# Kernel optimization log

Measured on AMD Instinct MI355X. Metric: run time of the kernel, lower is better.

The kernel has to match this reference:

```python
import jax, jax.numpy as jnp
import numpy as np

EPS = 1e-5
KS = 3
PAD = 1


def _bn(x, g, b, m, v):
    inv = g / jnp.sqrt(v + EPS)
    return x * inv[None, :, None, None] + (b - m * inv)[None, :, None, None]


def _deform_conv2d(x, off_w, off_b, w):
    # x: (B,C,H,W); off_w: (2*9,C,3,3); w: (Cout,C,3,3)
    B, C, H, W = x.shape
    N = KS * KS
    off = jax.lax.conv_general_dilated(x, off_w, (1, 1), ((PAD, PAD), (PAD, PAD)))
    off = off + off_b[None, :, None, None]                      # (B,2N,H,W)
    xp = jnp.pad(x, ((0, 0), (0, 0), (PAD, PAD), (PAD, PAD)))
    Hp, Wp = H + 2 * PAD, W + 2 * PAD
    r = jnp.arange(KS, dtype=x.dtype) - (KS - 1) // 2           # kernel offsets
    pny = jnp.repeat(r, KS)                                     # row-major (dy)
    pnx = jnp.tile(r, KS)                                       # row-major (dx)
    p0y = jnp.arange(1, H + 1, dtype=x.dtype)[None, None, :, None]
    p0x = jnp.arange(1, W + 1, dtype=x.dtype)[None, None, None, :]
    py = off[:, :N] + pny[None, :, None, None] + p0y            # (B,N,H,W)
    px = off[:, N:] + pnx[None, :, None, None] + p0x
    py = jnp.clip(py, 0.0, Hp - 1.0)
    px = jnp.clip(px, 0.0, Wp - 1.0)
    fy = jax.lax.stop_gradient(jnp.floor(py))                   # indices detached (as in torch impl)
    fx = jax.lax.stop_gradient(jnp.floor(px))
    qy0 = jnp.clip(fy, 0.0, Hp - 1.0)
    qx0 = jnp.clip(fx, 0.0, Wp - 1.0)
    qy1 = jnp.clip(fy + 1.0, 0.0, Hp - 1.0)
    qx1 = jnp.clip(fx + 1.0, 0.0, Wp - 1.0)
    xf = xp.reshape(B, C, Hp * Wp)

    def gather(qy, qx):
        idx = (qy * Wp + qx).astype(jnp.int32)                  # (B,N,H,W)
        return jax.vmap(lambda m_, i_: m_[:, i_])(xf, idx)       # (B,C,N,H,W)

    g_lt = (1.0 + (qy0 - py)) * (1.0 + (qx0 - px))
    g_rb = (1.0 - (qy1 - py)) * (1.0 - (qx1 - px))
    g_lb = (1.0 + (qy0 - py)) * (1.0 - (qx1 - px))
    g_rt = (1.0 - (qy1 - py)) * (1.0 + (qx0 - px))
    xo = (g_lt[:, None] * gather(qy0, qx0) + g_rb[:, None] * gather(qy1, qx1)
          + g_lb[:, None] * gather(qy0, qx1) + g_rt[:, None] * gather(qy1, qx0))
    # (B,C,N,H,W) -> (B,C,H*KS,W*KS): N = (row, col) row-major
    xo = xo.reshape(B, C, KS, KS, H, W).transpose(0, 1, 4, 2, 5, 3).reshape(B, C, H * KS, W * KS)
    return jax.lax.conv_general_dilated(xo, w, (KS, KS), 'VALID')


def _forward(x, dc1_offw, dc1_offb, dc1_w, bn1_g, bn1_b, bn1_m, bn1_v,
             dc2_offw, dc2_offb, dc2_w, bn2_g, bn2_b, bn2_m, bn2_v,
             id_w, id_b, bn3_g, bn3_b, bn3_m, bn3_v):
    h = jax.nn.relu(_bn(_deform_conv2d(x, dc1_offw, dc1_offb, dc1_w), bn1_g, bn1_b, bn1_m, bn1_v))
    h = _bn(_deform_conv2d(h, dc2_offw, dc2_offb, dc2_w), bn2_g, bn2_b, bn2_m, bn2_v)
    idt = jnp.einsum('bchw,oc->bohw', x, id_w[:, :, 0, 0]) + id_b[None, :, None, None]
    idt = _bn(idt, bn3_g, bn3_b, bn3_m, bn3_v)
    return jax.nn.relu(h + idt)


def setup_inputs() -> dict:
    key = jax.random.key(0)
    ks = jax.random.split(key, 16)
    B, Cin, Cout, H, W = 2, 64, 128, 128, 128
    N2 = 2 * KS * KS
    d = {}
    d['x'] = jax.random.normal(ks[0], (B, Cin, H, W), jnp.float32)
    d['dc1_offw'] = jax.random.normal(ks[1], (N2, Cin, KS, KS), jnp.float32) * 0.01
    d['dc1_offb'] = jnp.zeros((N2,), jnp.float32)
    d['dc1_w'] = jax.random.normal(ks[2], (Cout, Cin, KS, KS), jnp.float32) * 0.05
    d['bn1_g'] = 1.0 + 0.1 * jax.random.normal(ks[3], (Cout,), jnp.float32)
    d['bn1_b'] = 0.1 * jax.random.normal(ks[4], (Cout,), jnp.float32)
    d['bn1_m'] = 0.1 * jax.random.normal(ks[5], (Cout,), jnp.float32)
    d['bn1_v'] = jnp.ones((Cout,), jnp.float32)
    d['dc2_offw'] = jax.random.normal(ks[6], (N2, Cout, KS, KS), jnp.float32) * 0.01
    d['dc2_offb'] = jnp.zeros((N2,), jnp.float32)
    d['dc2_w'] = jax.random.normal(ks[7], (Cout, Cout, KS, KS), jnp.float32) * 0.03
    d['bn2_g'] = 1.0 + 0.1 * jax.random.normal(ks[8], (Cout,), jnp.float32)
    d['bn2_b'] = 0.1 * jax.random.normal(ks[9], (Cout,), jnp.float32)
    d['bn2_m'] = 0.1 * jax.random.normal(ks[10], (Cout,), jnp.float32)
    d['bn2_v'] = jnp.ones((Cout,), jnp.float32)
    d['id_w'] = jax.random.normal(ks[11], (Cout, Cin, 1, 1), jnp.float32) * 0.1
    d['id_b'] = jnp.zeros((Cout,), jnp.float32)
    d['bn3_g'] = 1.0 + 0.1 * jax.random.normal(ks[12], (Cout,), jnp.float32)
    d['bn3_b'] = 0.1 * jax.random.normal(ks[13], (Cout,), jnp.float32)
    d['bn3_m'] = 0.1 * jax.random.normal(ks[14], (Cout,), jnp.float32)
    d['bn3_v'] = jnp.ones((Cout,), jnp.float32)
    return d


def reference(x, dc1_offw, dc1_offb, dc1_w, bn1_g, bn1_b, bn1_m, bn1_v,
              dc2_offw, dc2_offb, dc2_w, bn2_g, bn2_b, bn2_m, bn2_v,
              id_w, id_b, bn3_g, bn3_b, bn3_m, bn3_v):
    return _forward(x, dc1_offw, dc1_offb, dc1_w, bn1_g, bn1_b, bn1_m, bn1_v,
                    dc2_offw, dc2_offb, dc2_w, bn2_g, bn2_b, bn2_m, bn2_v,
                    id_w, id_b, bn3_g, bn3_b, bn3_m, bn3_v)
```

## Files before the change

kernel.cpp:

```cpp
#include <hip/hip_runtime.h>
#include <math.h>

#define HH 128
#define WW 128
#define HWSZ (HH * WW)
#define BB 2
#define COUT 128

typedef __bf16 bf16x8 __attribute__((ext_vector_type(8)));
typedef float f32x4 __attribute__((ext_vector_type(4)));
typedef float f32x2 __attribute__((ext_vector_type(2)));
typedef short s16x8 __attribute__((ext_vector_type(8)));
typedef short s16x4 __attribute__((ext_vector_type(4)));
typedef unsigned short u16x4 __attribute__((ext_vector_type(4)));
typedef unsigned short u16x8 __attribute__((ext_vector_type(8)));

__device__ __forceinline__ short tobf(float f) {
  union { float f; unsigned u; } v; v.f = f;
  unsigned r = v.u + 0x7fffu + ((v.u >> 16) & 1u);
  return (short)(r >> 16);
}
__device__ __forceinline__ float asf(unsigned u) {
  union { unsigned u; float f; } v; v.u = u;
  return v.f;
}
__device__ __forceinline__ f32x2 up2(unsigned u) {
  f32x2 r; r[0] = asf(u << 16); r[1] = asf(u & 0xffff0000u); return r;
}
__device__ __forceinline__ unsigned trunc2bf(f32x2 v) {
  union { float f; unsigned u; } a, b;
  a.f = v[0]; b.f = v[1];
  return __builtin_amdgcn_perm(b.u, a.u, 0x07060302u);
}

#define PA0 73728
#define PA1 221184
#define PA2 229376
#define PA3 247808
#define PA4 284672
#define PA5 284928
__global__ __launch_bounds__(256) void prep_all_kernel(
    const float* __restrict__ dc1_w, const float* __restrict__ dc2_w,
    const float* __restrict__ id_w, const float* __restrict__ dc1_offw,
    const float* __restrict__ dc2_offw,
    const float* g1, const float* b1, const float* m1, const float* v1,
    const float* g2, const float* b2, const float* m2, const float* v2,
    const float* g3, const float* b3, const float* m3, const float* v3,
    const float* idb,
    short* __restrict__ wbf1, short* __restrict__ wbf2,
    short* __restrict__ woff1, short* __restrict__ woff2,
    float* __restrict__ cb1, float* __restrict__ cb2) {
  int idx = blockIdx.x * 256 + threadIdx.x;
  if (idx < PA0) {
    int o = idx / 576, k = idx - o * 576;
    float inv = g1[o] / sqrtf(v1[o] + 1e-5f);
    int col = (k % 9) * 64 + k / 9;
    int di = (((col >> 5) * 2 + (o >> 6)) * 4 + ((o >> 4) & 3)) * 512
           + (((o & 15) | (((col >> 3) & 3) << 4)) * 8) + (col & 7);
    wbf1[di] = tobf(dc1_w[(size_t)o * 576 + k] * inv);
  } else if (idx < PA1) {
    int j = idx - PA0;
    int o = j / 1152, k = j - o * 1152;
    float inv = g2[o] / sqrtf(v2[o] + 1e-5f);
    int col = (k % 9) * 128 + k / 9;
    int di = (((col >> 5) * 2 + (o >> 6)) * 4 + ((o >> 4) & 3)) * 512
           + (((o & 15) | (((col >> 3) & 3) << 4)) * 8) + (col & 7);
    wbf2[di] = tobf(dc2_w[(size_t)o * 1152 + k] * inv);
  } else if (idx < PA2) {
    int j = idx - PA1;
    int o = j >> 6, k = j & 63;
    float inv = g3[o] / sqrtf(v3[o] + 1e-5f);
    int col = 1152 + k;
    int di = (((col >> 5) * 2 + (o >> 6)) * 4 + ((o >> 4) & 3)) * 512
           + (((o & 15) | (((col >> 3) & 3) << 4)) * 8) + (col & 7);
    wbf2[di] = tobf(id_w[(size_t)o * 64 + k] * inv);
  } else if (idx < PA3) {
    int j = idx - PA2;
    int o = j / 576, k = j - o * 576;
    int col = (k % 9) * 64 + k / 9;
    int di = ((col >> 5) * 2 + (o >> 4)) * 512 + ((col >> 3) & 3) * 128
           + (o & 15) * 8 + (col & 7);
    woff1[di] = (o < 18) ? tobf(dc1_offw[(size_t)o * 576 + k]) : (short)0;
  } else if (idx < PA4) {
    int j = idx - PA3;
    int o = j / 1152, k = j - o * 1152;
    int col = (k % 9) * 128 + k / 9;
    int di = ((col >> 5) * 2 + (o >> 4)) * 512 + ((col >> 3) & 3) * 128
           + (o & 15) * 8 + (col & 7);
    woff2[di] = (o < 18) ? tobf(dc2_offw[(size_t)o * 1152 + k]) : (short)0;
  } else if (idx < PA5) {
    int j = idx - PA4;
    if (j < 128) {
      float inv = g1[j] / sqrtf(v1[j] + 1e-5f);
      cb1[j] = b1[j] - m1[j] * inv;
    } else {
      int o = j - 128;
      float inv2_ = g2[o] / sqrtf(v2[o] + 1e-5f);
      float inv3_ = g3[o] / sqrtf(v3[o] + 1e-5f);
      cb2[o] = (b2[o] - m2[o] * inv2_) + idb[o] * inv3_ + (b3[o] - m3[o] * inv3_);
    }
  }
}

__global__ __launch_bounds__(256) void xcast_kernel(const float* __restrict__ x,
                                                    unsigned short* __restrict__ xn) {
  __shared__ short lds[64 * 72];
  int tid = threadIdx.x;
  int gp0 = blockIdx.x * 64;
  int b = gp0 >> 14;
  int pl0 = gp0 & 16383;
  int p = tid & 63;
  int cb = (tid >> 6) * 16;
#pragma unroll
  for (int i = 0; i < 16; i++) {
    int c = cb + i;
    lds[p * 72 + c] = tobf(x[((size_t)(b * 64 + c)) * HWSZ + pl0 + p]);
  }
  __syncthreads();
  int pw = tid >> 2, cseg = (tid & 3) * 16;
  u16x8 a = *(const u16x8*)&lds[pw * 72 + cseg];
  u16x8 b8 = *(const u16x8*)&lds[pw * 72 + cseg + 8];
  *(u16x8*)&xn[(size_t)(gp0 + pw) * 64 + cseg] = a;
  *(u16x8*)&xn[(size_t)(gp0 + pw) * 64 + cseg + 8] = b8;
}

#define LOADW(kc_)                                              \
  {                                                             \
    const short* wf_ = wfb + (size_t)(kc_) * 4096;              \
    w0 = *(const bf16x8*)(wf_);                                 \
    w1 = *(const bf16x8*)(wf_ + 512);                           \
    w2 = *(const bf16x8*)(wf_ + 1024);                          \
    w3 = *(const bf16x8*)(wf_ + 1536);                          \
    w4 = *(const bf16x8*)(wf_ + 2048);                          \
    w5 = *(const bf16x8*)(wf_ + 2560);                          \
    w6 = *(const bf16x8*)(wf_ + 3072);                          \
    w7 = *(const bf16x8*)(wf_ + 3584);                          \
  }

#define LOADD(kc_)                                              \
  {                                                             \
    int n_ = ((kc_) << 5) >> CSH;                               \
    Dd0 = dsu[(n_ << 5) + dp];                                  \
  }

#define LOADG(P, kc_)                                           \
  {                                                             \
    int k0_ = (kc_) << 5;                                       \
    int c0_ = (k0_ & (Cin - 1)) + cq * 8;                       \
    int dx_ = (int)(Dd0.w & 0xffffu);                           \
    int dy_ = (int)Dd0.w >> 16;                                 \
    const unsigned short* p_ = inb + (int)Dd0.z + c0_;          \
    P##q00 = *(const uint4*)(p_);                               \
    P##q01 = *(const uint4*)(p_ + dx_);                         \
    P##q02 = *(const uint4*)(p_ + dy_);                         \
    P##q03 = *(const uint4*)(p_ + dx_ + dy_);                   \
    P##wa0 = Dd0.x; P##wb0 = Dd0.y;                             \
  }

#define BLEND1(r0, r1, r2, r3, wav, wbv, pkv)                                 \
  {                                                                           \
    float w0_ = asf((wav) << 16), w1_ = asf((wav) & 0xffff0000u);             \
    float w2_ = asf((wbv) << 16), w3_ = asf((wbv) & 0xffff0000u);             \
    f32x2 v0_ = up2(r0.x) * w0_ + up2(r1.x) * w1_                             \
              + up2(r2.x) * w2_ + up2(r3.x) * w3_;                            \
    f32x2 v1_ = up2(r0.y) * w0_ + up2(r1.y) * w1_                             \
              + up2(r2.y) * w2_ + up2(r3.y) * w3_;                            \
    f32x2 v2_ = up2(r0.z) * w0_ + up2(r1.z) * w1_                             \
              + up2(r2.z) * w2_ + up2(r3.z) * w3_;                            \
    f32x2 v3_ = up2(r0.w) * w0_ + up2(r1.w) * w1_                             \
              + up2(r2.w) * w2_ + up2(r3.w) * w3_;                            \
    pkv.x = trunc2bf(v0_); pkv.y = trunc2bf(v1_);                             \
    pkv.z = trunc2bf(v2_); pkv.w = trunc2bf(v3_);                             \
  }

#define XPOSE(pkv, bfrv)                                                      \
  {                                                                           \
    union { int i[4]; bf16x8 v; } bu_;                                        \
    bu_.i[0] = __builtin_amdgcn_ds_bpermute(baddr, (int)pkv.x);               \
    bu_.i[1] = __builtin_amdgcn_ds_bpermute(baddr, (int)pkv.y);               \
    bu_.i[2] = __builtin_amdgcn_ds_bpermute(baddr, (int)pkv.z);               \
    bu_.i[3] = __builtin_amdgcn_ds_bpermute(baddr, (int)pkv.w);               \
    bfrv = bu_.v;                                                             \
  }

#define MFMA8(bfr0v)                                                                \
  {                                                                                 \
    acc[0] = __builtin_amdgcn_mfma_f32_16x16x32_bf16(w0, bfr0v, acc[0], 0, 0, 0);   \
    acc[1] = __builtin_amdgcn_mfma_f32_16x16x32_bf16(w1, bfr0v, acc[1], 0, 0, 0);   \
    acc[2] = __builtin_amdgcn_mfma_f32_16x16x32_bf16(w2, bfr0v, acc[2], 0, 0, 0);   \
    acc[3] = __builtin_amdgcn_mfma_f32_16x16x32_bf16(w3, bfr0v, acc[3], 0, 0, 0);   \
    acc[4] = __builtin_amdgcn_mfma_f32_16x16x32_bf16(w4, bfr0v, acc[4], 0, 0, 0);   \
    acc[5] = __builtin_amdgcn_mfma_f32_16x16x32_bf16(w5, bfr0v, acc[5], 0, 0, 0);   \
    acc[6] = __builtin_amdgcn_mfma_f32_16x16x32_bf16(w6, bfr0v, acc[6], 0, 0, 0);   \
    acc[7] = __builtin_amdgcn_mfma_f32_16x16x32_bf16(w7, bfr0v, acc[7], 0, 0, 0);   \
  }

#define COMPUTE(P)                                                            \
  {                                                                           \
    uint4 pk0_;                                                               \
    BLEND1(P##q00, P##q01, P##q02, P##q03, P##wa0, P##wb0, pk0_);             \
    bf16x8 bf0_;                                                              \
    XPOSE(pk0_, bf0_);                                                        \
    __builtin_amdgcn_s_setprio(1);                                            \
    MFMA8(bf0_);                                                              \
    __builtin_amdgcn_s_setprio(0);                                            \
  }

template <int CSH, int KCONV, int KTOT, int MODE>
__global__ __launch_bounds__(256, 3) void fused_layer_kernel(
    const unsigned short* __restrict__ in, const short* __restrict__ woff,
    const float* __restrict__ offb,
    const short* __restrict__ wbf, const float* __restrict__ cbv,
    const unsigned short* __restrict__ xid, float* __restrict__ outf,
    unsigned short* __restrict__ outb) {
  __shared__ __align__(16) char smem[25088];
  uint4* dsu = (uint4*)smem;
  f32x4* redf = (f32x4*)smem;
  float* offlds = (float*)(smem + 16384);
  short* trans = (short*)(smem + 16384);

  const int tid = threadIdx.x;
  const int lane = tid & 63, wv = tid >> 6;
  const int pb = ((blockIdx.x & 7) << 7) | (blockIdx.x >> 3);
  const int pix0 = pb << 5;
  const int pl = pix0 & 16383;
  const int x0 = pl & 127, y = pl >> 7, b = pix0 >> 14;
  constexpr int Cin = 1 << CSH;
  const unsigned short* inb = in + (size_t)b * HWSZ * Cin;
  const int l15 = lane & 15, quad = lane >> 4;
  const int pxa = wv & 1, kh = wv >> 1;
  const int dp = pxa * 16 + (lane >> 2);
  const int cq = lane & 3;
  const int baddr = (((lane & 15) << 2) | (lane >> 4)) << 2;

  if (wv < 2) {
    constexpr int NCh = (9 << CSH) >> 5;
    const int pxga = wv;
    const int px = x0 + pxga * 16 + l15;
    f32x4 aco0 = {0.f, 0.f, 0.f, 0.f};
    f32x4 aco1 = {0.f, 0.f, 0.f, 0.f};
#pragma unroll
    for (int i = 0; i < NCh; i++) {
      int k0 = i * 32;
      int n = k0 >> CSH;
      int c0 = (k0 & (Cin - 1)) + quad * 8;
      int yy = y + n / 3 - 1;
      int xx = px + n % 3 - 1;
      bf16x8 bv = {};
      if (((unsigned)yy < (unsigned)HH) && ((unsigned)xx < (unsigned)WW))
        bv = *(const bf16x8*)&inb[((size_t)yy * WW + xx) * Cin + c0];
      int fbase = i * 1024 + lane * 8;
      bf16x8 a0 = *(const bf16x8*)&woff[fbase];
      bf16x8 a1 = *(const bf16x8*)&woff[fbase + 512];
      aco0 = __builtin_amdgcn_mfma_f32_16x16x32_bf16(a0, bv, aco0, 0, 0, 0);
      aco1 = __builtin_amdgcn_mfma_f32_16x16x32_bf16(a1, bv, aco1, 0, 0, 0);
    }
#pragma unroll
    for (int r = 0; r < 4; r++) {
      int o0 = quad * 4 + r;
      offlds[o0 * 32 + pxga * 16 + l15] = aco0[r] + offb[o0];
      int o1 = 16 + quad * 4 + r;
      if (o1 < 18)
        offlds[o1 * 32 + pxga * 16 + l15] = aco1[r] + offb[o1];
    }
  }

  bf16x8 w0, w1, w2, w3, w4, w5, w6, w7;
  uint4 Aq00, Aq01, Aq02, Aq03;
  uint4 Bq00, Bq01, Bq02, Bq03;
  unsigned Awa0, Awb0, Bwa0, Bwb0;
  uint4 Dd0;

  constexpr int NC = KTOT >> 5;
  constexpr int NCONV = KCONV >> 5;
  const int kcBeg = (NC * kh) >> 1;
  const int kcEnd = (NC * (kh + 1)) >> 1;
  const int kcEndConv = (kcEnd < NCONV) ? kcEnd : NCONV;
  const short* wfb = wbf + lane * 8;

  __syncthreads();

  for (int t = tid; t < 288; t += 256) {
    int n = t >> 5, pp = t & 31;
    float offy = offlds[n * 32 + pp];
    float offx = offlds[(9 + n) * 32 + pp];
    float py = offy + (float)(n / 3 - 1) + (float)(y + 1);
    float px = offx + (float)(n % 3 - 1) + (float)(x0 + pp + 1);
    py = fminf(fmaxf(py, 0.f), 129.f);
    px = fminf(fmaxf(px, 0.f), 129.f);
    float fy = floorf(py), fx = floorf(px);
    float qy1 = fminf(fy + 1.f, 129.f), qx1 = fminf(fx + 1.f, 129.f);
    float ty0 = 1.f + fy - py, ty1 = 1.f - (qy1 - py);
    float tx0 = 1.f + fx - px, tx1 = 1.f - (qx1 - px);
    int iy0 = (int)fy - 1, ix0 = (int)fx - 1;
    int iy1 = (int)qy1 - 1, ix1 = (int)qx1 - 1;
    if ((unsigned)iy0 >= (unsigned)HH) ty0 = 0.f;
    if ((unsigned)iy1 >= (unsigned)HH) ty1 = 0.f;
    if ((unsigned)ix0 >= (unsigned)WW) tx0 = 0.f;
    if ((unsigned)ix1 >= (unsigned)WW) tx1 = 0.f;
    int by0 = min(max(iy0, 0), HH - 1), by1 = min(max(iy1, 0), HH - 1);
    int bx0 = min(max(ix0, 0), WW - 1), bx1 = min(max(ix1, 0), WW - 1);
    uint4 d4;
    d4.x = (unsigned)(unsigned short)tobf(ty0 * tx0)
         | ((unsigned)(unsigned short)tobf(ty0 * tx1) << 16);
    d4.y = (unsigned)(unsigned short)tobf(ty1 * tx0)
         | ((unsigned)(unsigned short)tobf(ty1 * tx1) << 16);
    d4.z = (unsigned)((by0 * WW + bx0) * Cin);
    d4.w = (unsigned)((((by1 - by0) * WW * Cin) << 16) | ((bx1 - bx0) * Cin));
    dsu[t] = d4;
  }

  f32x4 acc[8];
#pragma unroll
  for (int j = 0; j < 8; j++) acc[j] = (f32x4){0.f, 0.f, 0.f, 0.f};

  __syncthreads();

  int i = kcBeg;
  if (i < kcEndConv) {
    const int kcLast = kcEndConv - 1;
    LOADD(i);
    LOADG(A, i);
    LOADD(min(i + 1, kcLast));
    for (; i + 2 <= kcEndConv; i += 2) {
      LOADW(i);
      LOADG(B, i + 1);
      LOADD(min(i + 2, kcLast));
      COMPUTE(A);
      LOADW(i + 1);
      if (i + 2 < kcEndConv) {
        LOADG(A, i + 2);
        LOADD(min(i + 3, kcLast));
      }
      COMPUTE(B);
    }
    if (i < kcEndConv) {
      LOADW(i);
      COMPUTE(A);
      i++;
    }
  }

  if (KCONV < KTOT) {
    for (; i < kcEnd; i++) {
      LOADW(i);
      int c = ((i << 5) - KCONV) + cq * 8;
      uint4 pk0 = *(const uint4*)&xid[((size_t)(b * HWSZ) + y * WW + x0 + dp) * 64 + c];
      bf16x8 bf0;
      XPOSE(pk0, bf0);
      __builtin_amdgcn_s_setprio(1);
      MFMA8(bf0);
      __builtin_amdgcn_s_setprio(0);
    }
  }

  __syncthreads();
  if (kh == 1) {
#pragma unroll
    for (int f = 0; f < 8; f++) redf[(f * 2 + pxa) * 64 + lane] = acc[f];
  }
  __syncthreads();
  if (kh == 0) {
#pragma unroll
    for (int f = 0; f < 8; f++) acc[f] += redf[(f * 2 + pxa) * 64 + lane];
    if (MODE == 1) {
#pragma unroll
      for (int f = 0; f < 8; f++) {
        int px_ = x0 + pxa * 16 + l15;
#pragma unroll
        for (int r = 0; r < 4; r++) {
          int o = (f >> 2) * 64 + (f & 3) * 16 + quad * 4 + r;
          outf[(size_t)(b * COUT + o) * HWSZ + y * WW + px_] =
              fmaxf(acc[f][r] + cbv[o], 0.f);
        }
      }
    } else {
#pragma unroll
      for (int f = 0; f < 8; f++) {
        int pl_ = pxa * 16 + l15;
        s16x4 t4;
#pragma unroll
        for (int r = 0; r < 4; r++) {
          int o = (f >> 2) * 64 + (f & 3) * 16 + quad * 4 + r;
          t4[r] = tobf(fmaxf(acc[f][r] + cbv[o], 0.f));
        }
        *(s16x4*)&trans[pl_ * 136 + (f >> 2) * 64 + (f & 3) * 16 + quad * 4] = t4;
      }
    }
  }
  if (MODE == 0) {
    __syncthreads();
    int pw = tid >> 3, cs = (tid & 7) * 16;
    size_t gb = ((size_t)(b * HWSZ) + y * WW + x0 + pw) * 128 + cs;
#pragma unroll
    for (int s = 0; s < 2; s++) {
      u16x8 v8 = *(const u16x8*)&trans[pw * 136 + cs + s * 8];
      *(u16x8*)&outb[gb + s * 8] = v8;
    }
  }
}

extern "C" void kernel_launch(void* const* d_in, const int* in_sizes, int n_in,
                              void* d_out, int out_size, void* d_ws, size_t ws_size,
                              hipStream_t stream) {
  const float* x        = (const float*)d_in[0];
  const float* dc1_offw = (const float*)d_in[1];
  const float* dc1_offb = (const float*)d_in[2];
  const float* dc1_w    = (const float*)d_in[3];
  const float* bn1_g    = (const float*)d_in[4];
  const float* bn1_b    = (const float*)d_in[5];
  const float* bn1_m    = (const float*)d_in[6];
  const float* bn1_v    = (const float*)d_in[7];
  const float* dc2_offw = (const float*)d_in[8];
  const float* dc2_offb = (const float*)d_in[9];
  const float* dc2_w    = (const float*)d_in[10];
  const float* bn2_g    = (const float*)d_in[11];
  const float* bn2_b    = (const float*)d_in[12];
  const float* bn2_m    = (const float*)d_in[13];
  const float* bn2_v    = (const float*)d_in[14];
  const float* id_w     = (const float*)d_in[15];
  const float* id_b     = (const float*)d_in[16];
  const float* bn3_g    = (const float*)d_in[17];
  const float* bn3_b    = (const float*)d_in[18];
  const float* bn3_m    = (const float*)d_in[19];
  const float* bn3_v    = (const float*)d_in[20];

  float* wsf = (float*)d_ws;
  float* cb1  = wsf;
  float* cb2  = cb1 + 128;
  unsigned short* xbf = (unsigned short*)(cb2 + 128);
  unsigned short* h1  = xbf + (size_t)BB * HWSZ * 64;
  short* wbf1  = (short*)(h1 + (size_t)BB * HWSZ * COUT);
  short* wbf2  = wbf1 + (size_t)128 * 576;
  short* woff1 = wbf2 + (size_t)128 * 1216;
  short* woff2 = woff1 + (size_t)18 * 1024;

  hipLaunchKernelGGL(prep_all_kernel, dim3((PA5 + 255) / 256), dim3(256), 0, stream,
                     dc1_w, dc2_w, id_w, dc1_offw, dc2_offw,
                     bn1_g, bn1_b, bn1_m, bn1_v, bn2_g, bn2_b, bn2_m, bn2_v,
                     bn3_g, bn3_b, bn3_m, bn3_v, id_b,
                     wbf1, wbf2, woff1, woff2, cb1, cb2);
  hipLaunchKernelGGL(xcast_kernel, dim3(BB * HWSZ / 64), dim3(256), 0, stream, x, xbf);

  hipLaunchKernelGGL((fused_layer_kernel<6, 576, 576, 0>), dim3(1024), dim3(256), 0, stream,
                     xbf, woff1, dc1_offb, wbf1, cb1,
                     (const unsigned short*)nullptr, (float*)nullptr, h1);
  hipLaunchKernelGGL((fused_layer_kernel<7, 1152, 1216, 1>), dim3(1024), dim3(256), 0, stream,
                     h1, woff2, dc2_offb, wbf2, cb2,
                     xbf, (float*)d_out, (unsigned short*)nullptr);
}
```

Measured before the change: 188.8 us.

## Triple-buffer deformable gather loads in conv main loop

Replaces the two-stage A/B register double buffering of gathered input samples with a three-stage A/B/C rotation, so gathers run two chunks ahead of the MFMA compute. The K-split between the two halves changes so each half gets exactly half of the conv chunks, with the identity tail going to the second half. The intent is to hide gather latency better. The cost is higher register pressure, and the loop requires the chunk count per half to be a multiple of three or the remainder is silently dropped.

Measured after the change: 186.9 us. About the same (-1.0%).

```diff
diff --git a/kernel.cpp b/kernel.cpp
--- a/kernel.cpp
+++ b/kernel.cpp
@@ -268,14 +268,16 @@
   bf16x8 w0, w1, w2, w3, w4, w5, w6, w7;
   uint4 Aq00, Aq01, Aq02, Aq03;
   uint4 Bq00, Bq01, Bq02, Bq03;
-  unsigned Awa0, Awb0, Bwa0, Bwb0;
+  uint4 Cq00, Cq01, Cq02, Cq03;
+  unsigned Awa0, Awb0, Bwa0, Bwb0, Cwa0, Cwb0;
   uint4 Dd0;
 
   constexpr int NC = KTOT >> 5;
   constexpr int NCONV = KCONV >> 5;
-  const int kcBeg = (NC * kh) >> 1;
-  const int kcEnd = (NC * (kh + 1)) >> 1;
-  const int kcEndConv = (kcEnd < NCONV) ? kcEnd : NCONV;
+  constexpr int HC = NCONV >> 1;
+  const int kcBeg = kh * HC;
+  const int kcEndConv = kcBeg + HC;
+  const int kcEnd = (kh == 1) ? NC : kcEndConv;
   const short* wfb = wbf + lane * 8;
 
   __syncthreads();
@@ -317,27 +319,26 @@
   __syncthreads();
 
   int i = kcBeg;
-  if (i < kcEndConv) {
-    const int kcLast = kcEndConv - 1;
+  {
+    const int last = kcEndConv - 1;
     LOADD(i);
     LOADG(A, i);
-    LOADD(min(i + 1, kcLast));
-    for (; i + 2 <= kcEndConv; i += 2) {
-      LOADW(i);
-      LOADG(B, i + 1);
-      LOADD(min(i + 2, kcLast));
-      COMPUTE(A);
-      LOADW(i + 1);
-      if (i + 2 < kcEndConv) {
-        LOADG(A, i + 2);
-        LOADD(min(i + 3, kcLast));
-      }
-      COMPUTE(B);
-    }
-    if (i < kcEndConv) {
+    LOADD(min(i + 1, last));
+    LOADG(B, min(i + 1, last));
+    LOADD(min(i + 2, last));
+    for (; i + 3 <= kcEndConv; i += 3) {
+      LOADG(C, min(i + 2, last));
+      LOADD(min(i + 3, last));
       LOADW(i);
       COMPUTE(A);
-      i++;
+      LOADG(A, min(i + 3, last));
+      LOADD(min(i + 4, last));
+      LOADW(i + 1);
+      COMPUTE(B);
+      LOADG(B, min(i + 4, last));
+      LOADD(min(i + 5, last));
+      LOADW(i + 2);
+      COMPUTE(C);
     }
   }
 
```
